# Performance work log

Measured on AMD Instinct MI355X. Metric: run time of the kernel, lower is better.

The kernel has to match this reference:

```python
import jax, jax.numpy as jnp
import numpy as np
from math import sqrt

B, NQ, NK = 16, 1024, 1024
DIM_Q = DIM_K = DIM_V = 512
H = 8
EPS = 1e-5


def _layernorm(x, gamma, beta):
    mu = jnp.mean(x, axis=-1, keepdims=True)
    var = jnp.mean(jnp.square(x - mu), axis=-1, keepdims=True)
    return (x - mu) * jax.lax.rsqrt(var + EPS) * gamma + beta


def setup_inputs() -> dict:
    key = jax.random.key(0)
    ks = jax.random.split(key, 12)
    s = 0.02
    return {
        "Q": jax.random.normal(ks[0], (B, NQ, DIM_Q), jnp.float32),
        "K": jax.random.normal(ks[1], (B, NK, DIM_K), jnp.float32),
        "Wq": jax.random.normal(ks[2], (DIM_Q, DIM_V), jnp.float32) * s,
        "bq": jnp.zeros((DIM_V,), jnp.float32),
        "Wk": jax.random.normal(ks[3], (DIM_K, DIM_V), jnp.float32) * s,
        "bk": jnp.zeros((DIM_V,), jnp.float32),
        "Wv": jax.random.normal(ks[4], (DIM_K, DIM_V), jnp.float32) * s,
        "bv": jnp.zeros((DIM_V,), jnp.float32),
        "Wo": jax.random.normal(ks[5], (DIM_V, DIM_V), jnp.float32) * s,
        "bo": jnp.zeros((DIM_V,), jnp.float32),
        "g0": jnp.ones((DIM_V,), jnp.float32),
        "b0": jnp.zeros((DIM_V,), jnp.float32),
        "g1": jnp.ones((DIM_V,), jnp.float32),
        "b1": jnp.zeros((DIM_V,), jnp.float32),
    }


def reference(Q, K, Wq, bq, Wk, bk, Wv, bv, Wo, bo, g0, b0, g1, b1):
    d = DIM_V // H  # head dim
    q = (Q @ Wq + bq).reshape(B, NQ, H, d)
    k = (K @ Wk + bk).reshape(B, NK, H, d)
    v = (K @ Wv + bv).reshape(B, NK, H, d)
    # NOTE: original scales by sqrt(dim_V), not sqrt(head_dim)
    scores = jnp.einsum("bqhd,bkhd->bhqk", q, k) / sqrt(DIM_V)
    A = jax.nn.softmax(scores, axis=-1)
    attn = jnp.einsum("bhqk,bkhd->bqhd", A, v)
    O = (q + attn).reshape(B, NQ, DIM_V)  # residual is post-projection q
    O = _layernorm(O, g0, b0)
    O = O + jax.nn.relu(O @ Wo + bo)
    O = _layernorm(O, g1, b1)
    return O
```

## Files before the change

### kernel.cpp

```cpp
#include <hip/hip_runtime.h>
#include <hip/hip_bf16.h>

typedef __attribute__((ext_vector_type(8))) short short8;
typedef __attribute__((ext_vector_type(4))) float f32x4;
typedef __attribute__((ext_vector_type(4))) float float4v;
typedef __attribute__((ext_vector_type(4))) unsigned short ushort4v;
typedef __attribute__((ext_vector_type(4))) unsigned int uint4v;

#define MFMA16(a, b, c) __builtin_amdgcn_mfma_f32_16x16x32_bf16((a), (b), (c), 0, 0, 0)

__device__ __forceinline__ unsigned short f2bf(float f) {
    union { float f; unsigned u; } v; v.f = f;
    unsigned r = v.u + 0x7fffu + ((v.u >> 16) & 1u);
    return (unsigned short)(r >> 16);
}
__device__ __forceinline__ float bf2f(unsigned short h) {
    union { unsigned u; float f; } v; v.u = (unsigned)h << 16;
    return v.f;
}
__device__ __forceinline__ unsigned cvt_pk_bf16(float lo, float hi) {
    unsigned r;
    asm("v_cvt_pk_bf16_f32 %0, %1, %2" : "=v"(r) : "v"(lo), "v"(hi));
    return r;
}
__device__ __forceinline__ void gl16(const void* g, void* l) {
    __builtin_amdgcn_global_load_lds(
        (const __attribute__((address_space(1))) unsigned int*)g,
        (__attribute__((address_space(3))) unsigned int*)l, 16, 0, 0);
}

__global__ __launch_bounds__(256) void cvt_kernel(
    const float* __restrict__ Q, const float* __restrict__ K,
    unsigned short* __restrict__ Qb, unsigned short* __restrict__ Kb)
{
    const float* in = blockIdx.z ? K : Q;
    unsigned short* out = blockIdx.z ? Kb : Qb;
    size_t i = ((size_t)blockIdx.x * 256 + threadIdx.x) * 8;
    float4v v0 = *(const float4v*)(in + i);
    float4v v1 = *(const float4v*)(in + i + 4);
    short8 o;
#pragma unroll
    for (int j = 0; j < 4; ++j) { o[j] = (short)f2bf(v0[j]); o[4 + j] = (short)f2bf(v1[j]); }
    size_t row7 = (i >> 9) & 7;
    *(short8*)(out + (i ^ (row7 << 3))) = o;
}

__global__ __launch_bounds__(256) void wtrans_kernel(
    const float* __restrict__ W0, const float* __restrict__ W1,
    const float* __restrict__ W2, const float* __restrict__ W3,
    unsigned short* __restrict__ T0, unsigned short* __restrict__ T1,
    unsigned short* __restrict__ T2, unsigned short* __restrict__ T3)
{
    const int z = blockIdx.z;
    const float* W = (z == 0) ? W0 : (z == 1) ? W1 : (z == 2) ? W2 : W3;
    unsigned short* T = (z == 0) ? T0 : (z == 1) ? T1 : (z == 2) ? T2 : T3;

    __shared__ unsigned short tile[64][72];
    const int k0 = blockIdx.x * 64, n0 = blockIdx.y * 64;
    const int t = threadIdx.x;

#pragma unroll
    for (int p = 0; p < 4; ++p) {
        int idx = p * 256 + t;
        int k = idx >> 4, c4 = idx & 15;
        float4v v = *(const float4v*)(W + (size_t)(k0 + k) * 512 + n0 + c4 * 4);
#pragma unroll
        for (int j = 0; j < 4; ++j) tile[k][c4 * 4 + j] = f2bf(v[j]);
    }
    __syncthreads();
#pragma unroll
    for (int p = 0; p < 2; ++p) {
        int idx = p * 256 + t;
        int n = idx >> 3, c = idx & 7;
        short8 o;
#pragma unroll
        for (int j = 0; j < 8; ++j) o[j] = (short)tile[c * 8 + j][n];
        *(short8*)(T + (size_t)(n0 + n) * 512 + k0 + ((c ^ (n & 7)) * 8)) = o;
    }
}

__global__ __launch_bounds__(256) void proj_kernel(
    const unsigned short* __restrict__ Qb, const unsigned short* __restrict__ Kb,
    const unsigned short* __restrict__ WqT, const unsigned short* __restrict__ WkT,
    const unsigned short* __restrict__ WvT,
    const float* __restrict__ bq, const float* __restrict__ bk, const float* __restrict__ bv,
    unsigned short* __restrict__ qb, unsigned short* __restrict__ kb,
    unsigned short* __restrict__ vT)
{
    const int z = blockIdx.z;
    const unsigned short* A = (z == 0) ? Qb : Kb;
    const unsigned short* WT = (z == 0) ? WqT : (z == 1) ? WkT : WvT;
    const float* bias = (z == 0) ? bq : (z == 1) ? bk : bv;

    __shared__ unsigned short Al[128 * 64];
    __shared__ unsigned short Bl[128 * 64];

    const int t = threadIdx.x;
    const int lane = t & 63, wid = t >> 6;
    const int wm = wid >> 1, wn = wid & 1;
    const int l15 = lane & 15, grp = lane >> 4;
    const int rowbase = blockIdx.y * 128;
    const int colbase = blockIdx.x * 128;
    const int srow = t >> 3, sblk = t & 7;

    f32x4 acc[4][4];
#pragma unroll
    for (int i = 0; i < 4; ++i)
#pragma unroll
        for (int j = 0; j < 4; ++j) acc[i][j] = (f32x4){0.f, 0.f, 0.f, 0.f};

    for (int kt = 0; kt < 8; ++kt) {
#pragma unroll
        for (int p = 0; p < 4; ++p)
            gl16(A + (size_t)(rowbase + p * 32 + srow) * 512 + kt * 64 + sblk * 8,
                 &Al[p * 2048 + wid * 512]);
#pragma unroll
        for (int p = 0; p < 4; ++p)
            gl16(WT + (size_t)(colbase + p * 32 + srow) * 512 + kt * 64 + sblk * 8,
                 &Bl[p * 2048 + wid * 512]);
        __syncthreads();
#pragma unroll
        for (int kk = 0; kk < 2; ++kk) {
            short8 af[4], bfr[4];
#pragma unroll
            for (int m = 0; m < 4; ++m) {
                int r = wm * 64 + m * 16 + l15;
                af[m] = *(const short8*)((const char*)Al + r * 128 + (((kk * 4 + grp) ^ (r & 7)) << 4));
            }
#pragma unroll
            for (int n = 0; n < 4; ++n) {
                int r = wn * 64 + n * 16 + l15;
                bfr[n] = *(const short8*)((const char*)Bl + r * 128 + (((kk * 4 + grp) ^ (r & 7)) << 4));
            }
#pragma unroll
            for (int m = 0; m < 4; ++m)
#pragma unroll
                for (int n = 0; n < 4; ++n)
                    acc[m][n] = MFMA16(af[m], bfr[n], acc[m][n]);
        }
        __syncthreads();
    }

    if (z == 2) {
#pragma unroll
        for (int n = 0; n < 4; ++n) {
            int col = colbase + wn * 64 + n * 16 + l15;
            float bvv = bias[col];
            int h_ = col >> 6, d_ = col & 63;
#pragma unroll
            for (int m = 0; m < 4; ++m) {
                int row0 = rowbase + wm * 64 + m * 16 + grp * 4;
                int b_ = row0 >> 10;
                int key0 = row0 & 1023;
                int keypos = (key0 & ~63) + ((((key0 >> 3) & 7) ^ (d_ & 7)) << 3) + (key0 & 7);
                ushort4v w;
#pragma unroll
                for (int r = 0; r < 4; ++r) w[r] = f2bf(acc[m][n][r] + bvv);
                *(ushort4v*)(vT + ((size_t)(b_ * 8 + h_) * 64 + d_) * 1024 + keypos) = w;
            }
        }
    } else if (z == 1) {
#pragma unroll
        for (int n = 0; n < 4; ++n) {
            int col = colbase + wn * 64 + n * 16 + l15;
            float bvv = bias[col];
#pragma unroll
            for (int m = 0; m < 4; ++m) {
                int row0 = rowbase + wm * 64 + m * 16 + grp * 4;
#pragma unroll
                for (int r = 0; r < 4; ++r) {
                    int row = row0 + r;
                    int k6 = row & 63;
                    int y = ((k6 & 4) << 3) | ((k6 & 56) >> 1) | (k6 & 3);
                    int Y = (row & ~63) | y;
                    int colp = col ^ ((y & 7) << 3);
                    kb[(size_t)Y * 512 + colp] = f2bf(acc[m][n][r] + bvv);
                }
            }
        }
    } else {
#pragma unroll
        for (int n = 0; n < 4; ++n) {
            int col = colbase + wn * 64 + n * 16 + l15;
            float bvv = bias[col];
#pragma unroll
            for (int m = 0; m < 4; ++m) {
                int row0 = rowbase + wm * 64 + m * 16 + grp * 4;
#pragma unroll
                for (int r = 0; r < 4; ++r)
                    qb[(size_t)(row0 + r) * 512 + col] = f2bf(acc[m][n][r] + bvv);
            }
        }
    }
}

__global__ __launch_bounds__(256, 4) void attn_kernel(
    const unsigned short* __restrict__ qb, const unsigned short* __restrict__ kbs,
    const unsigned short* __restrict__ vTs, unsigned short* __restrict__ Opre)
{
    __shared__ unsigned short Kl[2][64 * 64];
    __shared__ unsigned short Vl[2][64 * 64];

    const int t = threadIdx.x, lane = t & 63, wid = t >> 6;
    const int l15 = lane & 15, grp = lane >> 4;

    const int bid = blockIdx.x;
    const int h = bid & 7, r2 = bid >> 3;
    const int b = r2 >> 3, qt = r2 & 7;
    const int qbase = qt * 128 + wid * 32;

    const unsigned short* ksrc = kbs + (size_t)(b * 1024 + (t >> 3)) * 512 + h * 64 + (t & 7) * 8;
    const unsigned short* vsrc = vTs + ((size_t)(b * 8 + h) * 64 + (t >> 3)) * 1024 + (t & 7) * 8;

#define STAGE(bsel, tile) do { \
    gl16(ksrc + (size_t)((tile) * 64) * 512,      &Kl[bsel][wid * 512]); \
    gl16(ksrc + (size_t)((tile) * 64 + 32) * 512, &Kl[bsel][2048 + wid * 512]); \
    gl16(vsrc + (tile) * 64,                      &Vl[bsel][wid * 512]); \
    gl16(vsrc + 32768 + (tile) * 64,              &Vl[bsel][2048 + wid * 512]); } while (0)

    short8 qfrag[2][2];
#pragma unroll
    for (int qf = 0; qf < 2; ++qf)
#pragma unroll
        for (int kk = 0; kk < 2; ++kk)
            qfrag[qf][kk] = *(const short8*)(
                qb + (size_t)(b * 1024 + qbase + qf * 16 + l15) * 512 + h * 64 + kk * 32 + grp * 8);

    f32x4 o[2][4];
#pragma unroll
    for (int qf = 0; qf < 2; ++qf)
#pragma unroll
        for (int df = 0; df < 4; ++df) o[qf][df] = (f32x4){0.f, 0.f, 0.f, 0.f};
    float mrun[2] = {0.f, 0.f}, lrun[2] = {0.f, 0.f};

    const float C = 0.06375871f;

    STAGE(0, 0);
    __syncthreads();

    for (int kt = 0; kt < 16; ++kt) {
        const int buf = kt & 1;
        if (kt < 15) STAGE(buf ^ 1, kt + 1);

        const char* Kb_ = (const char*)&Kl[buf][0];
        const char* Vb_ = (const char*)&Vl[buf][0];

        f32x4 s[2][4];
#pragma unroll
        for (int qf = 0; qf < 2; ++qf)
#pragma unroll
            for (int nf = 0; nf < 4; ++nf) s[qf][nf] = (f32x4){0.f, 0.f, 0.f, 0.f};
        __builtin_amdgcn_s_setprio(1);
#pragma unroll
        for (int kk = 0; kk < 2; ++kk) {
            short8 kf[4];
#pragma unroll
            for (int nf = 0; nf < 4; ++nf) {
                int r = nf * 16 + l15;
                kf[nf] = *(const short8*)(Kb_ + r * 128 + (((kk * 4 + grp) ^ (r & 7)) << 4));
            }
#pragma unroll
            for (int qf = 0; qf < 2; ++qf)
#pragma unroll
                for (int nf = 0; nf < 4; ++nf)
                    s[qf][nf] = MFMA16(kf[nf], qfrag[qf][kk], s[qf][nf]);
        }
        __builtin_amdgcn_s_setprio(0);

        short8 pa[2][2];
#pragma unroll
        for (int qf = 0; qf < 2; ++qf) {
            float a0 = fmaxf(fmaxf(s[qf][0][0], s[qf][0][1]), fmaxf(s[qf][0][2], s[qf][0][3]));
            float a1 = fmaxf(fmaxf(s[qf][1][0], s[qf][1][1]), fmaxf(s[qf][1][2], s[qf][1][3]));
            float a2 = fmaxf(fmaxf(s[qf][2][0], s[qf][2][1]), fmaxf(s[qf][2][2], s[qf][2][3]));
            float a3 = fmaxf(fmaxf(s[qf][3][0], s[qf][3][1]), fmaxf(s[qf][3][2], s[qf][3][3]));
            float lm = fmaxf(fmaxf(a0, a1), fmaxf(a2, a3));
            if (__any((lm - mrun[qf]) * C > 8.f)) {
                float mr = lm;
                mr = fmaxf(mr, __shfl_xor(mr, 16));
                mr = fmaxf(mr, __shfl_xor(mr, 32));
                float mnew = fmaxf(mrun[qf], mr);
                float rs = __builtin_amdgcn_exp2f((mrun[qf] - mnew) * C);
                mrun[qf] = mnew;
                lrun[qf] *= rs;
#pragma unroll
                for (int df = 0; df < 4; ++df)
#pragma unroll
                    for (int r = 0; r < 4; ++r) o[qf][df][r] *= rs;
            }
            float nmc = -mrun[qf] * C;
            float p[4][4];
            float ls = 0.f;
#pragma unroll
            for (int nf = 0; nf < 4; ++nf)
#pragma unroll
                for (int r = 0; r < 4; ++r) {
                    p[nf][r] = __builtin_amdgcn_exp2f(fmaf(s[qf][nf][r], C, nmc));
                    ls += p[nf][r];
                }
            lrun[qf] += ls;
            union { uint4v u; short8 s8; } c0, c1;
            c0.u[0] = cvt_pk_bf16(p[0][0], p[0][1]);
            c0.u[1] = cvt_pk_bf16(p[0][2], p[0][3]);
            c0.u[2] = cvt_pk_bf16(p[2][0], p[2][1]);
            c0.u[3] = cvt_pk_bf16(p[2][2], p[2][3]);
            c1.u[0] = cvt_pk_bf16(p[1][0], p[1][1]);
            c1.u[1] = cvt_pk_bf16(p[1][2], p[1][3]);
            c1.u[2] = cvt_pk_bf16(p[3][0], p[3][1]);
            c1.u[3] = cvt_pk_bf16(p[3][2], p[3][3]);
            pa[qf][0] = c0.s8;
            pa[qf][1] = c1.s8;
        }

        __builtin_amdgcn_s_setprio(1);
#pragma unroll
        for (int kk = 0; kk < 2; ++kk)
#pragma unroll
            for (int df = 0; df < 4; ++df) {
                int r = df * 16 + l15;
                short8 vf = *(const short8*)(Vb_ + r * 128 + (((kk * 4 + grp) ^ (r & 7)) << 4));
#pragma unroll
                for (int qf = 0; qf < 2; ++qf)
                    o[qf][df] = MFMA16(vf, pa[qf][kk], o[qf][df]);
            }
        __builtin_amdgcn_s_setprio(0);
        __syncthreads();
    }
#undef STAGE

#pragma unroll
    for (int qf = 0; qf < 2; ++qf) {
        float l = lrun[qf];
        l += __shfl_xor(l, 16);
        l += __shfl_xor(l, 32);
        float linv = 1.f / l;
        size_t row = (size_t)(b * 1024 + qbase + qf * 16 + l15);
#pragma unroll
        for (int df = 0; df < 4; ++df) {
            int col = h * 64 + df * 16 + grp * 4;
            ushort4v res = *(const ushort4v*)(qb + row * 512 + col);
            ushort4v outv;
#pragma unroll
            for (int r = 0; r < 4; ++r)
                outv[r] = f2bf(o[qf][df][r] * linv + bf2f(res[r]));
            *(ushort4v*)(Opre + row * 512 + col) = outv;
        }
    }
}

template <int OUT_F32>
__global__ __launch_bounds__(256) void ln_kernel(
    const unsigned short* in, const float* __restrict__ g, const float* __restrict__ be,
    unsigned short* outb, float* outf)
{
    const int wid = threadIdx.x >> 6, lane = threadIdx.x & 63;
    const size_t row = (size_t)blockIdx.x * 4 + wid;
    short8 v = *(const short8*)(in + row * 512 + lane * 8);
    float x[8];
    float sum = 0.f, sq = 0.f;
#pragma unroll
    for (int j = 0; j < 8; ++j) {
        x[j] = bf2f((unsigned short)v[j]);
        sum += x[j];
        sq += x[j] * x[j];
    }
#pragma unroll
    for (int ofs = 1; ofs < 64; ofs <<= 1) {
        sum += __shfl_xor(sum, ofs);
        sq += __shfl_xor(sq, ofs);
    }
    float mean = sum * (1.f / 512.f);
    float var = sq * (1.f / 512.f) - mean * mean;
    float rs = rsqrtf(var + 1e-5f);
    float4v g0 = *(const float4v*)(g + lane * 8);
    float4v g1 = *(const float4v*)(g + lane * 8 + 4);
    float4v b0 = *(const float4v*)(be + lane * 8);
    float4v b1 = *(const float4v*)(be + lane * 8 + 4);
    float y[8];
#pragma unroll
    for (int j = 0; j < 4; ++j) y[j] = (x[j] - mean) * rs * g0[j] + b0[j];
#pragma unroll
    for (int j = 0; j < 4; ++j) y[4 + j] = (x[4 + j] - mean) * rs * g1[j] + b1[j];
    if (OUT_F32) {
        float4v o0, o1;
#pragma unroll
        for (int j = 0; j < 4; ++j) { o0[j] = y[j]; o1[j] = y[4 + j]; }
        *(float4v*)(outf + row * 512 + lane * 8) = o0;
        *(float4v*)(outf + row * 512 + lane * 8 + 4) = o1;
    } else {
        short8 o;
#pragma unroll
        for (int j = 0; j < 8; ++j) o[j] = (short)f2bf(y[j]);
        size_t op = row * 512 + (size_t)((lane >> 3) * 64 + (((lane & 7) ^ ((int)row & 7)) * 8));
        *(short8*)(outb + op) = o;
    }
}

__global__ __launch_bounds__(256) void ffn_kernel(
    const unsigned short* __restrict__ O1, const unsigned short* __restrict__ WoT,
    const float* __restrict__ bo, unsigned short* __restrict__ O2)
{
    __shared__ unsigned short Al[128 * 64];
    __shared__ unsigned short Bl[128 * 64];

    const int t = threadIdx.x;
    const int lane = t & 63, wid = t >> 6;
    const int wm = wid >> 1, wn = wid & 1;
    const int l15 = lane & 15, grp = lane >> 4;
    const int rowbase = blockIdx.y * 128;
    const int colbase = blockIdx.x * 128;
    const int srow = t >> 3, sblk = t & 7;

    f32x4 acc[4][4];
#pragma unroll
    for (int i = 0; i < 4; ++i)
#pragma unroll
        for (int j = 0; j < 4; ++j) acc[i][j] = (f32x4){0.f, 0.f, 0.f, 0.f};

    for (int kt = 0; kt < 8; ++kt) {
#pragma unroll
        for (int p = 0; p < 4; ++p)
            gl16(O1 + (size_t)(rowbase + p * 32 + srow) * 512 + kt * 64 + sblk * 8,
                 &Al[p * 2048 + wid * 512]);
#pragma unroll
        for (int p = 0; p < 4; ++p)
            gl16(WoT + (size_t)(colbase + p * 32 + srow) * 512 + kt * 64 + sblk * 8,
                 &Bl[p * 2048 + wid * 512]);
        __syncthreads();
#pragma unroll
        for (int kk = 0; kk < 2; ++kk) {
            short8 af[4], bfr[4];
#pragma unroll
            for (int m = 0; m < 4; ++m) {
                int r = wm * 64 + m * 16 + l15;
                af[m] = *(const short8*)((const char*)Al + r * 128 + (((kk * 4 + grp) ^ (r & 7)) << 4));
            }
#pragma unroll
            for (int n = 0; n < 4; ++n) {
                int r = wn * 64 + n * 16 + l15;
                bfr[n] = *(const short8*)((const char*)Bl + r * 128 + (((kk * 4 + grp) ^ (r & 7)) << 4));
            }
#pragma unroll
            for (int m = 0; m < 4; ++m)
#pragma unroll
                for (int n = 0; n < 4; ++n)
                    acc[m][n] = MFMA16(af[m], bfr[n], acc[m][n]);
        }
        __syncthreads();
    }
#pragma unroll
    for (int n = 0; n < 4; ++n) {
        int col = colbase + wn * 64 + n * 16 + l15;
        float bvv = bo[col];
#pragma unroll
        for (int m = 0; m < 4; ++m) {
            int row0 = rowbase + wm * 64 + m * 16 + grp * 4;
#pragma unroll
            for (int r = 0; r < 4; ++r) {
                size_t row = (size_t)(row0 + r);
                float val = fmaxf(acc[m][n][r] + bvv, 0.f);
                float resid = bf2f(O1[row * 512 + (col ^ (((int)row & 7) << 3))]);
                O2[row * 512 + col] = f2bf(resid + val);
            }
        }
    }
}

extern "C" void kernel_launch(void* const* d_in, const int* in_sizes, int n_in,
                              void* d_out, int out_size, void* d_ws, size_t ws_size,
                              hipStream_t stream)
{
    const float* Q   = (const float*)d_in[0];
    const float* Kin = (const float*)d_in[1];
    const float* Wq  = (const float*)d_in[2];
    const float* bq  = (const float*)d_in[3];
    const float* Wk  = (const float*)d_in[4];
    const float* bk  = (const float*)d_in[5];
    const float* Wv  = (const float*)d_in[6];
    const float* bv  = (const float*)d_in[7];
    const float* Wo  = (const float*)d_in[8];
    const float* bo  = (const float*)d_in[9];
    const float* g0  = (const float*)d_in[10];
    const float* b0  = (const float*)d_in[11];
    const float* g1  = (const float*)d_in[12];
    const float* b1  = (const float*)d_in[13];
    float* out = (float*)d_out;

    unsigned short* ws = (unsigned short*)d_ws;
    const size_t WSZ = 512 * 512;
    const size_t BIG = 16384 * 512;
    unsigned short* WqT  = ws;
    unsigned short* WkT  = WqT + WSZ;
    unsigned short* WvT  = WkT + WSZ;
    unsigned short* WoT  = WvT + WSZ;
    unsigned short* qb   = WoT + WSZ;
    unsigned short* kb   = qb + BIG;
    unsigned short* vT   = kb + BIG;
    unsigned short* Opre = vT + BIG;
    unsigned short* Qbf  = Opre + BIG;
    unsigned short* Kbf  = Qbf + BIG;
    unsigned short* O1   = Opre;
    unsigned short* O2   = Qbf;

    cvt_kernel<<<dim3(4096, 1, 2), 256, 0, stream>>>(Q, Kin, Qbf, Kbf);
    wtrans_kernel<<<dim3(8, 8, 4), 256, 0, stream>>>(Wq, Wk, Wv, Wo, WqT, WkT, WvT, WoT);
    proj_kernel<<<dim3(4, 128, 3), 256, 0, stream>>>(Qbf, Kbf, WqT, WkT, WvT, bq, bk, bv, qb, kb, vT);
    attn_kernel<<<dim3(1024), 256, 0, stream>>>(qb, kb, vT, Opre);
    ln_kernel<0><<<dim3(4096), 256, 0, stream>>>(Opre, g0, b0, O1, nullptr);
    ffn_kernel<<<dim3(4, 128), 256, 0, stream>>>(O1, WoT, bo, O2);
    ln_kernel<1><<<dim3(4096), 256, 0, stream>>>(O2, g1, b1, nullptr, out);
}
```

Baseline: 152.7 us.

## Triple-buffer K/V tiles and prescale Q by softmax constant

Switches the attention kernel's K/V LDS staging from double to triple buffering, prefetching two tiles ahead with explicit vmcnt waits and barriers instead of __syncthreads. Q fragments are prescaled by the log2-domain softmax constant once up front, which removes the per-element FMA in the exponent and adds a branch that skips the subtraction while the running max is zero. LDS use per block grows, which may reduce occupancy under the 4-blocks-per-CU bound. Rounding Q*C back to bf16 adds a small extra precision loss.

```diff
diff --git a/kernel.cpp b/kernel.cpp
--- a/kernel.cpp
+++ b/kernel.cpp
@@ -16,6 +16,10 @@
 }
 __device__ __forceinline__ float bf2f(unsigned short h) {
     union { unsigned u; float f; } v; v.u = (unsigned)h << 16;
+    return v.f;
+}
+__device__ __forceinline__ float asf(unsigned u) {
+    union { unsigned u; float f; } v; v.u = u;
     return v.f;
 }
 __device__ __forceinline__ unsigned cvt_pk_bf16(float lo, float hi) {
@@ -198,8 +202,8 @@
     const unsigned short* __restrict__ qb, const unsigned short* __restrict__ kbs,
     const unsigned short* __restrict__ vTs, unsigned short* __restrict__ Opre)
 {
-    __shared__ unsigned short Kl[2][64 * 64];
-    __shared__ unsigned short Vl[2][64 * 64];
+    __shared__ unsigned short Kl[3][64 * 64];
+    __shared__ unsigned short Vl[3][64 * 64];
 
     const int t = threadIdx.x, lane = t & 63, wid = t >> 6;
     const int l15 = lane & 15, grp = lane >> 4;
@@ -218,6 +222,8 @@
     gl16(vsrc + (tile) * 64,                      &Vl[bsel][wid * 512]); \
     gl16(vsrc + 32768 + (tile) * 64,              &Vl[bsel][2048 + wid * 512]); } while (0)
 
+    const float C = 0.06375871f;
+
     short8 qfrag[2][2];
 #pragma unroll
     for (int qf = 0; qf < 2; ++qf)
@@ -226,6 +232,25 @@
             qfrag[qf][kk] = *(const short8*)(
                 qb + (size_t)(b * 1024 + qbase + qf * 16 + l15) * 512 + h * 64 + kk * 32 + grp * 8);
 
+    STAGE(0, 0);
+    STAGE(1, 1);
+
+#pragma unroll
+    for (int qf = 0; qf < 2; ++qf)
+#pragma unroll
+        for (int kk = 0; kk < 2; ++kk) {
+            union { short8 s; uint4v u; } io;
+            io.s = qfrag[qf][kk];
+#pragma unroll
+            for (int j = 0; j < 4; ++j) {
+                unsigned w = io.u[j];
+                float flo = asf(w << 16) * C;
+                float fhi = asf(w & 0xffff0000u) * C;
+                io.u[j] = cvt_pk_bf16(flo, fhi);
+            }
+            qfrag[qf][kk] = io.s;
+        }
+
     f32x4 o[2][4];
 #pragma unroll
     for (int qf = 0; qf < 2; ++qf)
@@ -233,14 +258,12 @@
         for (int df = 0; df < 4; ++df) o[qf][df] = (f32x4){0.f, 0.f, 0.f, 0.f};
     float mrun[2] = {0.f, 0.f}, lrun[2] = {0.f, 0.f};
 
-    const float C = 0.06375871f;
-
-    STAGE(0, 0);
-    __syncthreads();
-
+    asm volatile("s_waitcnt vmcnt(4) lgkmcnt(0)" ::: "memory");
+    __builtin_amdgcn_s_barrier();
+
+    int buf = 0, nbuf = 2;
     for (int kt = 0; kt < 16; ++kt) {
-        const int buf = kt & 1;
-        if (kt < 15) STAGE(buf ^ 1, kt + 1);
+        if (kt < 14) STAGE(nbuf, kt + 2);
 
         const char* Kb_ = (const char*)&Kl[buf][0];
         const char* Vb_ = (const char*)&Vl[buf][0];
@@ -275,12 +298,12 @@
             float a2 = fmaxf(fmaxf(s[qf][2][0], s[qf][2][1]), fmaxf(s[qf][2][2], s[qf][2][3]));
             float a3 = fmaxf(fmaxf(s[qf][3][0], s[qf][3][1]), fmaxf(s[qf][3][2], s[qf][3][3]));
             float lm = fmaxf(fmaxf(a0, a1), fmaxf(a2, a3));
-            if (__any((lm - mrun[qf]) * C > 8.f)) {
+            if (__any(lm - mrun[qf] > 8.f)) {
                 float mr = lm;
                 mr = fmaxf(mr, __shfl_xor(mr, 16));
                 mr = fmaxf(mr, __shfl_xor(mr, 32));
                 float mnew = fmaxf(mrun[qf], mr);
-                float rs = __builtin_amdgcn_exp2f((mrun[qf] - mnew) * C);
+                float rs = __builtin_amdgcn_exp2f(mrun[qf] - mnew);
                 mrun[qf] = mnew;
                 lrun[qf] *= rs;
 #pragma unroll
@@ -288,17 +311,26 @@
 #pragma unroll
                     for (int r = 0; r < 4; ++r) o[qf][df][r] *= rs;
             }
-            float nmc = -mrun[qf] * C;
             float p[4][4];
-            float ls = 0.f;
-#pragma unroll
-            for (int nf = 0; nf < 4; ++nf)
-#pragma unroll
-                for (int r = 0; r < 4; ++r) {
-                    p[nf][r] = __builtin_amdgcn_exp2f(fmaf(s[qf][nf][r], C, nmc));
-                    ls += p[nf][r];
-                }
-            lrun[qf] += ls;
+            const float mq = mrun[qf];
+            if (mq == 0.f) {
+#pragma unroll
+                for (int nf = 0; nf < 4; ++nf)
+#pragma unroll
+                    for (int r = 0; r < 4; ++r)
+                        p[nf][r] = __builtin_amdgcn_exp2f(s[qf][nf][r]);
+            } else {
+#pragma unroll
+                for (int nf = 0; nf < 4; ++nf)
+#pragma unroll
+                    for (int r = 0; r < 4; ++r)
+                        p[nf][r] = __builtin_amdgcn_exp2f(s[qf][nf][r] - mq);
+            }
+            float t0 = (p[0][0] + p[0][1]) + (p[0][2] + p[0][3]);
+            float t1 = (p[1][0] + p[1][1]) + (p[1][2] + p[1][3]);
+            float t2 = (p[2][0] + p[2][1]) + (p[2][2] + p[2][3]);
+            float t3 = (p[3][0] + p[3][1]) + (p[3][2] + p[3][3]);
+            lrun[qf] += (t0 + t1) + (t2 + t3);
             union { uint4v u; short8 s8; } c0, c1;
             c0.u[0] = cvt_pk_bf16(p[0][0], p[0][1]);
             c0.u[1] = cvt_pk_bf16(p[0][2], p[0][3]);
@@ -324,7 +356,16 @@
                     o[qf][df] = MFMA16(vf, pa[qf][kk], o[qf][df]);
             }
         __builtin_amdgcn_s_setprio(0);
-        __syncthreads();
+
+        if (kt < 14) {
+            asm volatile("s_waitcnt vmcnt(4) lgkmcnt(0)" ::: "memory");
+            __builtin_amdgcn_s_barrier();
+        } else if (kt == 14) {
+            asm volatile("s_waitcnt vmcnt(0) lgkmcnt(0)" ::: "memory");
+            __builtin_amdgcn_s_barrier();
+        }
+        buf = (buf == 2) ? 0 : buf + 1;
+        nbuf = (nbuf == 2) ? 0 : nbuf + 1;
     }
 #undef STAGE
 
```

New measurement: 164.7 us. +7.8%, slower.
